# Optimization experiments

Hardware: AMD Instinct MI355X
Metric: run time of the kernel (lower is better)

## Reference

```python
import jax, jax.numpy as jnp
import numpy as np

B, K, D, S, E = 256, 512, 64, 100000, 20000  # batch, knowledge_n, low_dim, student_n, exer_n


def setup_inputs() -> dict:
    key = jax.random.key(0)
    ks = jax.random.split(key, 10)
    stu_id = jax.random.randint(ks[0], (B,), 0, S)
    exer_id = jax.random.randint(ks[1], (B,), 0, E)
    kn_emb = jax.random.uniform(ks[2], (B, K), dtype=jnp.float32)
    # learned parameters (xavier-ish scale)
    stu_table = jax.random.normal(ks[3], (S, D), dtype=jnp.float32) * 0.05
    exer_table = jax.random.normal(ks[4], (E, D), dtype=jnp.float32) * 0.05
    kn_table = jax.random.normal(ks[5], (K, D), dtype=jnp.float32) * 0.05
    W1 = jax.random.normal(ks[6], (K, K + D), dtype=jnp.float32) * (2.0 / (2 * K + D)) ** 0.5
    W2 = jax.random.normal(ks[7], (K, K + D), dtype=jnp.float32) * (2.0 / (2 * K + D)) ** 0.5
    W3 = jax.random.normal(ks[8], (1, K), dtype=jnp.float32) * (2.0 / (K + 1)) ** 0.5
    b3 = jnp.zeros((1,), dtype=jnp.float32)
    return {"stu_id": stu_id, "exer_id": exer_id, "kn_emb": kn_emb,
            "stu_table": stu_table, "exer_table": exer_table, "kn_table": kn_table,
            "W1": W1, "W2": W2, "W3": W3, "b3": b3}


def reference(stu_id, exer_id, kn_emb, stu_table, exer_table, kn_table, W1, W2, W3, b3):
    k = kn_table.shape[0]  # knowledge_n
    # sigmoid(stu_emb @ kn_table.T): (B, K) per-concept proficiency / difficulty
    stu = jax.nn.sigmoid(stu_table[stu_id] @ kn_table.T)
    exer = jax.nn.sigmoid(exer_table[exer_id] @ kn_table.T)
    # Linear on cat([repeated stu/exer vec, kn_vector]) decomposes: split W into
    # the first K columns (acting on the batch vector, constant over the K axis)
    # and the last D columns (acting on kn_table, constant over batch).
    pref = jax.nn.sigmoid((stu @ W1[:, :k].T)[:, None, :] + (kn_table @ W1[:, k:].T)[None, :, :])  # (B,K,K)
    diff = jax.nn.sigmoid((exer @ W2[:, :k].T)[:, None, :] + (kn_table @ W2[:, k:].T)[None, :, :])  # (B,K,K)
    o = jax.nn.sigmoid(jnp.einsum('bkn,n->bk', pref - diff, W3[0]) + b3)  # (B,K)
    sum_out = jnp.sum(o * kn_emb, axis=1, keepdims=True)  # (B,1)
    count = jnp.sum(kn_emb, axis=1, keepdims=True)
    return sum_out / count
```

## Files before the change

kernel.cpp:

```cpp
#include <hip/hip_runtime.h>

#define B_ 256
#define K_ 512
#define D_ 64
#define KD_ 576
#define LOG2E 1.44269504088896340736f

typedef float v2f __attribute__((ext_vector_type(2)));
typedef float v4f __attribute__((ext_vector_type(4)));
typedef short bf16x8 __attribute__((ext_vector_type(8)));
typedef float f32x16 __attribute__((ext_vector_type(16)));

#define ZERO16 {0.f,0.f,0.f,0.f,0.f,0.f,0.f,0.f,0.f,0.f,0.f,0.f,0.f,0.f,0.f,0.f}

__device__ __forceinline__ float fexp2(float x) {
#if __has_builtin(__builtin_amdgcn_exp2f)
    return __builtin_amdgcn_exp2f(x);
#else
    float r; asm("v_exp_f32 %0, %1" : "=v"(r) : "v"(x)); return r;
#endif
}
__device__ __forceinline__ float frcp(float x) {
#if __has_builtin(__builtin_amdgcn_rcpf)
    return __builtin_amdgcn_rcpf(x);
#else
    float r; asm("v_rcp_f32 %0, %1" : "=v"(r) : "v"(x)); return r;
#endif
}
__device__ __forceinline__ float fsig(float x) {
    return frcp(1.0f + fexp2(-LOG2E * x));
}
__device__ __forceinline__ ushort f2bf(float f) {
    union { float f; unsigned u; } v; v.f = f;
    return (ushort)((v.u + 0x7FFFu + ((v.u >> 16) & 1u)) >> 16);
}
__device__ __forceinline__ bf16x8 ldcvt8(const float* p) {
    float4 a = *(const float4*)p;
    float4 b = *(const float4*)(p + 4);
    bf16x8 r;
    r[0] = (short)f2bf(a.x); r[1] = (short)f2bf(a.y);
    r[2] = (short)f2bf(a.z); r[3] = (short)f2bf(a.w);
    r[4] = (short)f2bf(b.x); r[5] = (short)f2bf(b.y);
    r[6] = (short)f2bf(b.z); r[7] = (short)f2bf(b.w);
    return r;
}

__global__ void __launch_bounds__(256) kS(const int* __restrict__ sid,
                                          const int* __restrict__ eid,
                                          const float* __restrict__ stu_t,
                                          const float* __restrict__ exer_t,
                                          const float* __restrict__ kn_t,
                                          ushort* __restrict__ Sbu) {
    const int bid = blockIdx.x, t = threadIdx.x;
    const int l = t & 63, w = t >> 6;
    const int dk = (l >> 5) * 8;
    const int tab = bid >> 5, bt = (bid >> 3) & 3, nt = bid & 7;
    const int b0 = bt * 64, n0 = nt * 64;
    const int brow = b0 + (w & 1) * 32 + (l & 31);
    const int ncol = n0 + (w >> 1) * 32 + (l & 31);
    const int id = (tab ? eid : sid)[brow];
    const float* ar = (tab ? exer_t : stu_t) + (size_t)id * D_;
    const float* br = kn_t + (size_t)ncol * D_;
    f32x16 acc = ZERO16;
#pragma unroll
    for (int kk = 0; kk < 4; kk++) {
        bf16x8 a = ldcvt8(ar + kk * 16 + dk);
        bf16x8 b = ldcvt8(br + kk * 16 + dk);
        acc = __builtin_amdgcn_mfma_f32_32x32x16_bf16(a, b, acc, 0, 0, 0);
    }
    ushort* So = Sbu + (size_t)tab * B_ * K_;
#pragma unroll
    for (int r = 0; r < 16; r++) {
        const int row = (r & 3) + 8 * (r >> 2) + 4 * (l >> 5);
        So[(size_t)(b0 + (w & 1) * 32 + row) * K_ + ncol] = f2bf(fsig(acc[r]));
    }
}

__global__ void __launch_bounds__(256) kEF(const ushort* __restrict__ Sbu,
                                           const float* __restrict__ W1,
                                           const float* __restrict__ W2,
                                           const float* __restrict__ kn_t,
                                           float* __restrict__ E,
                                           float* __restrict__ FT1,
                                           float* __restrict__ FT2) {
    __shared__ float shm[4224];
    const int bid = blockIdx.x, t = threadIdx.x;
    const int l = t & 63, w = t >> 6;
    if (bid < 256) {
        const int mat = bid >> 7, bt = (bid >> 4) & 7, nt = bid & 15;
        const int b0 = bt * 32, n0 = nt * 32;
        const int arow = b0 + (l & 31);
        const int nrow = n0 + (l & 31);
        const int koff = w * 128 + (l >> 5) * 8;
        const short* Sp = (const short*)Sbu + (size_t)(mat * B_ + arow) * K_ + koff;
        const float* Wp = (mat ? W2 : W1) + (size_t)nrow * KD_ + koff;
        f32x16 acc = ZERO16;
#pragma unroll
        for (int kk = 0; kk < 8; kk++) {
            bf16x8 a = *(const bf16x8*)(Sp + kk * 16);
            bf16x8 b = ldcvt8(Wp + kk * 16);
            acc = __builtin_amdgcn_mfma_f32_32x32x16_bf16(a, b, acc, 0, 0, 0);
        }
#pragma unroll
        for (int r = 0; r < 16; r++) {
            const int row = (r & 3) + 8 * (r >> 2) + 4 * (l >> 5);
            shm[w * 1056 + row * 33 + (l & 31)] = acc[r];
        }
        __syncthreads();
#pragma unroll
        for (int i = 0; i < 4; i++) {
            const int o = i * 256 + t;
            const int row = (o >> 5) & 31, col = o & 31;
            const float v = shm[row * 33 + col] + shm[1056 + row * 33 + col]
                          + shm[2112 + row * 33 + col] + shm[3168 + row * 33 + col];
            E[(size_t)mat * B_ * K_ + (size_t)(b0 + row) * K_ + n0 + col]
                = fexp2(-LOG2E * v);
        }
    } else {
        const int fid = bid - 256;
        const int mat = fid >> 6, kt = (fid >> 3) & 7, nt = fid & 7;
        const int k0 = kt * 64, n0 = nt * 64;
        const int krow = k0 + (w & 1) * 32 + (l & 31);
        const int ncol = n0 + (w >> 1) * 32 + (l & 31);
        const int dk = (l >> 5) * 8;
        const float* Wm = mat ? W2 : W1;
        const float* ar = kn_t + (size_t)krow * D_;
        const float* br = Wm + (size_t)ncol * KD_ + K_;
        f32x16 acc = ZERO16;
#pragma unroll
        for (int kk = 0; kk < 4; kk++) {
            bf16x8 a = ldcvt8(ar + kk * 16 + dk);
            bf16x8 b = ldcvt8(br + kk * 16 + dk);
            acc = __builtin_amdgcn_mfma_f32_32x32x16_bf16(a, b, acc, 0, 0, 0);
        }
        const int nl_ = (w >> 1) * 32 + (l & 31);
#pragma unroll
        for (int r = 0; r < 16; r++) {
            const int row = (r & 3) + 8 * (r >> 2) + 4 * (l >> 5);
            shm[nl_ * 65 + (w & 1) * 32 + row] = fexp2(-LOG2E * acc[r]);
        }
        __syncthreads();
        float* Fo = mat ? FT2 : FT1;
#pragma unroll
        for (int i = 0; i < 16; i++) {
            const int q = i * 256 + t;
            const int r_ = q >> 6, c_ = q & 63;
            Fo[(size_t)(n0 + r_) * K_ + k0 + c_] = shm[r_ * 65 + c_];
        }
    }
}

__global__ void __launch_bounds__(512) kMain(const float* __restrict__ FT1,
                                             const float* __restrict__ FT2,
                                             const float* __restrict__ Ebase,
                                             const float* __restrict__ W3,
                                             float* __restrict__ pPart) {
    __shared__ float lds[4352];
    const int t = threadIdx.x;
    const int l = t & 63, w = t >> 6;
    const int kg = blockIdx.x, bg = blockIdx.y, ns = blockIdx.z;
    const int b0 = bg * 8;
    const int k = kg * 64 + l;

#pragma unroll
    for (int c = 0; c < 2; c++) {
        const int combo = w * 2 + c;
        const int mat = combo >> 3, b = combo & 7;
        const float* src = Ebase + (size_t)mat * B_ * K_ + (size_t)(b0 + b) * K_
                         + ns * 256;
#pragma unroll
        for (int j = 0; j < 4; j++) {
            const int nl = j * 64 + l;
            lds[mat * 2048 + nl * 8 + b] = src[nl];
        }
    }
    if (t < 256) lds[4096 + t] = W3[ns * 256 + t];
    __syncthreads();

    const int nbase = w * 32;
    const float* f1p = FT1 + (size_t)(ns * 256 + nbase) * K_ + k;
    const float* f2p = FT2 + (size_t)(ns * 256 + nbase) * K_ + k;

    v2f acc0 = {0.f, 0.f}, acc1 = {0.f, 0.f}, acc2 = {0.f, 0.f}, acc3 = {0.f, 0.f};

#pragma unroll 4
    for (int nl = 0; nl < 32; nl++) {
        const float f1 = f1p[(size_t)nl * K_];
        const float f2 = f2p[(size_t)nl * K_];
        const int n = nbase + nl;
        const float w3n = lds[4096 + n];
        const v4f e1a = *(const v4f*)&lds[n * 8];
        const v4f e1b = *(const v4f*)&lds[n * 8 + 4];
        const v4f e2a = *(const v4f*)&lds[2048 + n * 8];
        const v4f e2b = *(const v4f*)&lds[2048 + n * 8 + 4];
        {
            const v2f e1 = {e1a.x, e1a.y}, e2 = {e2a.x, e2a.y};
            const v2f pd = e1 * f1 + 1.0f, qd = e2 * f2 + 1.0f;
            const v2f den = pd * qd;
            v2f rc; rc.x = frcp(den.x); rc.y = frcp(den.y);
            acc0 += ((qd - pd) * w3n) * rc;
        }
        {
            const v2f e1 = {e1a.z, e1a.w}, e2 = {e2a.z, e2a.w};
            const v2f pd = e1 * f1 + 1.0f, qd = e2 * f2 + 1.0f;
            const v2f den = pd * qd;
            v2f rc; rc.x = frcp(den.x); rc.y = frcp(den.y);
            acc1 += ((qd - pd) * w3n) * rc;
        }
        {
            const v2f e1 = {e1b.x, e1b.y}, e2 = {e2b.x, e2b.y};
            const v2f pd = e1 * f1 + 1.0f, qd = e2 * f2 + 1.0f;
            const v2f den = pd * qd;
            v2f rc; rc.x = frcp(den.x); rc.y = frcp(den.y);
            acc2 += ((qd - pd) * w3n) * rc;
        }
        {
            const v2f e1 = {e1b.z, e1b.w}, e2 = {e2b.z, e2b.w};
            const v2f pd = e1 * f1 + 1.0f, qd = e2 * f2 + 1.0f;
            const v2f den = pd * qd;
            v2f rc; rc.x = frcp(den.x); rc.y = frcp(den.y);
            acc3 += ((qd - pd) * w3n) * rc;
        }
    }

    __syncthreads();
    {
        float* sa = lds + w * 512 + l * 8;
        *(v2f*)(sa + 0) = acc0;
        *(v2f*)(sa + 2) = acc1;
        *(v2f*)(sa + 4) = acc2;
        *(v2f*)(sa + 6) = acc3;
    }
    __syncthreads();
    float s = 0.f;
#pragma unroll
    for (int ww = 0; ww < 8; ww++) s += lds[ww * 512 + l * 8 + w];
    pPart[(((size_t)ns * 32 + bg) * 8 + w) * K_ + kg * 64 + l] = s;
}

__global__ void __launch_bounds__(256) kFin(const float* __restrict__ pPart,
                                            const float* __restrict__ kn_emb,
                                            const float* __restrict__ b3,
                                            float* __restrict__ out) {
    const int t = threadIdx.x, l = t & 63, w = t >> 6;
    const int b = blockIdx.x * 4 + w;
    const int bg = b >> 3, bi = b & 7;
    const float b3v = b3[0];
    const float* p0 = pPart + (((size_t)0 * 32 + bg) * 8 + bi) * K_;
    const float* p1 = pPart + (((size_t)1 * 32 + bg) * 8 + bi) * K_;
    const float* ke = kn_emb + (size_t)b * K_;
    float num = 0.f, den = 0.f;
#pragma unroll
    for (int c = 0; c < 8; c++) {
        const int kk = c * 64 + l;
        const float s = p0[kk] + p1[kk];
        const float kv = ke[kk];
        num = fmaf(fsig(s + b3v), kv, num);
        den += kv;
    }
#pragma unroll
    for (int off = 32; off; off >>= 1) {
        num += __shfl_xor(num, off, 64);
        den += __shfl_xor(den, off, 64);
    }
    if (l == 0) out[b] = num / den;
}

extern "C" void kernel_launch(void* const* d_in, const int* in_sizes, int n_in,
                              void* d_out, int out_size, void* d_ws, size_t ws_size,
                              hipStream_t stream) {
    const int*   stu_id     = (const int*)d_in[0];
    const int*   exer_id    = (const int*)d_in[1];
    const float* kn_emb     = (const float*)d_in[2];
    const float* stu_table  = (const float*)d_in[3];
    const float* exer_table = (const float*)d_in[4];
    const float* kn_table   = (const float*)d_in[5];
    const float* W1         = (const float*)d_in[6];
    const float* W2         = (const float*)d_in[7];
    const float* W3         = (const float*)d_in[8];
    const float* b3         = (const float*)d_in[9];
    float* out = (float*)d_out;

    float* ws = (float*)d_ws;
    float* FT1      = ws;
    float* FT2      = FT1 + (size_t)K_ * K_;
    float* E        = FT2 + (size_t)K_ * K_;
    ushort* Sbu     = (ushort*)(E + 2 * (size_t)B_ * K_);
    float* pPart    = (float*)(Sbu + 2 * (size_t)B_ * K_);

    kS<<<64, 256, 0, stream>>>(stu_id, exer_id, stu_table, exer_table,
                               kn_table, Sbu);
    kEF<<<384, 256, 0, stream>>>(Sbu, W1, W2, kn_table, E, FT1, FT2);
    kMain<<<dim3(8, 32, 2), 512, 0, stream>>>(FT1, FT2, E, W3, pPart);
    kFin<<<64, 256, 0, stream>>>(pPart, kn_emb, b3, out);
}
```

Baseline: 36.52 us.

## Fuse S and E GEMMs into one kernel and recompute F tiles inside main kernel

Result: slower. 46.18 us (+26.4%).

```diff
diff --git a/kernel.cpp b/kernel.cpp
--- a/kernel.cpp
+++ b/kernel.cpp
@@ -45,154 +45,139 @@
     return r;
 }
 
-__global__ void __launch_bounds__(256) kS(const int* __restrict__ sid,
-                                          const int* __restrict__ eid,
-                                          const float* __restrict__ stu_t,
-                                          const float* __restrict__ exer_t,
-                                          const float* __restrict__ kn_t,
-                                          ushort* __restrict__ Sbu) {
+__global__ void __launch_bounds__(256) kE2(const int* __restrict__ sid,
+                                           const int* __restrict__ eid,
+                                           const float* __restrict__ stu_t,
+                                           const float* __restrict__ exer_t,
+                                           const float* __restrict__ kn_t,
+                                           const float* __restrict__ W1,
+                                           const float* __restrict__ W2,
+                                           float* __restrict__ E) {
+    __shared__ ushort S_lds[32 * 512];
+    __shared__ float red[4 * 32 * 33];
+    __shared__ int ids[32];
     const int bid = blockIdx.x, t = threadIdx.x;
     const int l = t & 63, w = t >> 6;
-    const int dk = (l >> 5) * 8;
-    const int tab = bid >> 5, bt = (bid >> 3) & 3, nt = bid & 7;
-    const int b0 = bt * 64, n0 = nt * 64;
-    const int brow = b0 + (w & 1) * 32 + (l & 31);
-    const int ncol = n0 + (w >> 1) * 32 + (l & 31);
-    const int id = (tab ? eid : sid)[brow];
-    const float* ar = (tab ? exer_t : stu_t) + (size_t)id * D_;
-    const float* br = kn_t + (size_t)ncol * D_;
-    f32x16 acc = ZERO16;
-#pragma unroll
-    for (int kk = 0; kk < 4; kk++) {
-        bf16x8 a = ldcvt8(ar + kk * 16 + dk);
-        bf16x8 b = ldcvt8(br + kk * 16 + dk);
-        acc = __builtin_amdgcn_mfma_f32_32x32x16_bf16(a, b, acc, 0, 0, 0);
-    }
-    ushort* So = Sbu + (size_t)tab * B_ * K_;
-#pragma unroll
-    for (int r = 0; r < 16; r++) {
-        const int row = (r & 3) + 8 * (r >> 2) + 4 * (l >> 5);
-        So[(size_t)(b0 + (w & 1) * 32 + row) * K_ + ncol] = f2bf(fsig(acc[r]));
-    }
-}
-
-__global__ void __launch_bounds__(256) kEF(const ushort* __restrict__ Sbu,
-                                           const float* __restrict__ W1,
-                                           const float* __restrict__ W2,
-                                           const float* __restrict__ kn_t,
-                                           float* __restrict__ E,
-                                           float* __restrict__ FT1,
-                                           float* __restrict__ FT2) {
-    __shared__ float shm[4224];
-    const int bid = blockIdx.x, t = threadIdx.x;
-    const int l = t & 63, w = t >> 6;
-    if (bid < 256) {
-        const int mat = bid >> 7, bt = (bid >> 4) & 7, nt = bid & 15;
-        const int b0 = bt * 32, n0 = nt * 32;
-        const int arow = b0 + (l & 31);
-        const int nrow = n0 + (l & 31);
-        const int koff = w * 128 + (l >> 5) * 8;
-        const short* Sp = (const short*)Sbu + (size_t)(mat * B_ + arow) * K_ + koff;
-        const float* Wp = (mat ? W2 : W1) + (size_t)nrow * KD_ + koff;
+    const int mat = bid >> 7, bt = (bid >> 4) & 7, nt = bid & 15;
+    const int b0 = bt * 32, n0 = nt * 32;
+    if (t < 32) ids[t] = (mat ? eid : sid)[b0 + t];
+    __syncthreads();
+
+    {
+        const float* tab = mat ? exer_t : stu_t;
+        const float* ar = tab + (size_t)ids[l & 31] * D_ + (l >> 5) * 8;
+        const bf16x8 a0 = ldcvt8(ar),      a1 = ldcvt8(ar + 16),
+                     a2 = ldcvt8(ar + 32), a3 = ldcvt8(ar + 48);
+#pragma unroll
+        for (int tt = 0; tt < 4; tt++) {
+            const int ncol = w * 128 + tt * 32 + (l & 31);
+            const float* br = kn_t + (size_t)ncol * D_ + (l >> 5) * 8;
+            f32x16 acc = ZERO16;
+            acc = __builtin_amdgcn_mfma_f32_32x32x16_bf16(a0, ldcvt8(br),      acc, 0, 0, 0);
+            acc = __builtin_amdgcn_mfma_f32_32x32x16_bf16(a1, ldcvt8(br + 16), acc, 0, 0, 0);
+            acc = __builtin_amdgcn_mfma_f32_32x32x16_bf16(a2, ldcvt8(br + 32), acc, 0, 0, 0);
+            acc = __builtin_amdgcn_mfma_f32_32x32x16_bf16(a3, ldcvt8(br + 48), acc, 0, 0, 0);
+#pragma unroll
+            for (int r = 0; r < 16; r++) {
+                const int row = (r & 3) + 8 * (r >> 2) + 4 * (l >> 5);
+                const int byte = row * 1024 + ((ncol * 2) ^ ((row & 7) << 4));
+                *(ushort*)((char*)S_lds + byte) = f2bf(fsig(acc[r]));
+            }
+        }
+    }
+    __syncthreads();
+
+    {
+        const int row = l & 31;
+        const int swz = (row & 7) << 4;
+        const int kbase = w * 128 + (l >> 5) * 8;
+        const float* wr = (mat ? W2 : W1) + (size_t)(n0 + (l & 31)) * KD_ + kbase;
         f32x16 acc = ZERO16;
 #pragma unroll
         for (int kk = 0; kk < 8; kk++) {
-            bf16x8 a = *(const bf16x8*)(Sp + kk * 16);
-            bf16x8 b = ldcvt8(Wp + kk * 16);
+            const int kel = kbase + kk * 16;
+            bf16x8 a = *(const bf16x8*)((const char*)S_lds + row * 1024 + ((kel * 2) ^ swz));
+            bf16x8 b = ldcvt8(wr + kk * 16);
             acc = __builtin_amdgcn_mfma_f32_32x32x16_bf16(a, b, acc, 0, 0, 0);
         }
 #pragma unroll
         for (int r = 0; r < 16; r++) {
-            const int row = (r & 3) + 8 * (r >> 2) + 4 * (l >> 5);
-            shm[w * 1056 + row * 33 + (l & 31)] = acc[r];
-        }
-        __syncthreads();
-#pragma unroll
-        for (int i = 0; i < 4; i++) {
-            const int o = i * 256 + t;
-            const int row = (o >> 5) & 31, col = o & 31;
-            const float v = shm[row * 33 + col] + shm[1056 + row * 33 + col]
-                          + shm[2112 + row * 33 + col] + shm[3168 + row * 33 + col];
-            E[(size_t)mat * B_ * K_ + (size_t)(b0 + row) * K_ + n0 + col]
-                = fexp2(-LOG2E * v);
-        }
-    } else {
-        const int fid = bid - 256;
-        const int mat = fid >> 6, kt = (fid >> 3) & 7, nt = fid & 7;
-        const int k0 = kt * 64, n0 = nt * 64;
-        const int krow = k0 + (w & 1) * 32 + (l & 31);
-        const int ncol = n0 + (w >> 1) * 32 + (l & 31);
-        const int dk = (l >> 5) * 8;
-        const float* Wm = mat ? W2 : W1;
-        const float* ar = kn_t + (size_t)krow * D_;
-        const float* br = Wm + (size_t)ncol * KD_ + K_;
-        f32x16 acc = ZERO16;
-#pragma unroll
-        for (int kk = 0; kk < 4; kk++) {
-            bf16x8 a = ldcvt8(ar + kk * 16 + dk);
-            bf16x8 b = ldcvt8(br + kk * 16 + dk);
-            acc = __builtin_amdgcn_mfma_f32_32x32x16_bf16(a, b, acc, 0, 0, 0);
-        }
-        const int nl_ = (w >> 1) * 32 + (l & 31);
-#pragma unroll
-        for (int r = 0; r < 16; r++) {
-            const int row = (r & 3) + 8 * (r >> 2) + 4 * (l >> 5);
-            shm[nl_ * 65 + (w & 1) * 32 + row] = fexp2(-LOG2E * acc[r]);
-        }
-        __syncthreads();
-        float* Fo = mat ? FT2 : FT1;
-#pragma unroll
-        for (int i = 0; i < 16; i++) {
-            const int q = i * 256 + t;
-            const int r_ = q >> 6, c_ = q & 63;
-            Fo[(size_t)(n0 + r_) * K_ + k0 + c_] = shm[r_ * 65 + c_];
-        }
-    }
-}
-
-__global__ void __launch_bounds__(512) kMain(const float* __restrict__ FT1,
-                                             const float* __restrict__ FT2,
+            const int rowc = (r & 3) + 8 * (r >> 2) + 4 * (l >> 5);
+            red[w * 1056 + rowc * 33 + (l & 31)] = acc[r];
+        }
+    }
+    __syncthreads();
+#pragma unroll
+    for (int i = 0; i < 4; i++) {
+        const int o = i * 256 + t;
+        const int row = (o >> 5) & 31, col = o & 31;
+        const float v = red[row * 33 + col] + red[1056 + row * 33 + col]
+                      + red[2112 + row * 33 + col] + red[3168 + row * 33 + col];
+        E[(size_t)mat * B_ * K_ + (size_t)(b0 + row) * K_ + n0 + col]
+            = fexp2(-LOG2E * v);
+    }
+}
+
+__global__ void __launch_bounds__(512) kMain(const float* __restrict__ kn_t,
+                                             const float* __restrict__ W1,
+                                             const float* __restrict__ W2,
                                              const float* __restrict__ Ebase,
                                              const float* __restrict__ W3,
                                              float* __restrict__ pPart) {
-    __shared__ float lds[4352];
-    const int t = threadIdx.x;
-    const int l = t & 63, w = t >> 6;
+    __shared__ float lds[18816];
+    const int t = threadIdx.x, l = t & 63, w = t >> 6;
     const int kg = blockIdx.x, bg = blockIdx.y, ns = blockIdx.z;
     const int b0 = bg * 8;
-    const int k = kg * 64 + l;
-
-#pragma unroll
-    for (int c = 0; c < 2; c++) {
-        const int combo = w * 2 + c;
-        const int mat = combo >> 3, b = combo & 7;
-        const float* src = Ebase + (size_t)mat * B_ * K_ + (size_t)(b0 + b) * K_
-                         + ns * 256;
-#pragma unroll
-        for (int j = 0; j < 4; j++) {
-            const int nl = j * 64 + l;
-            lds[mat * 2048 + nl * 8 + b] = src[nl];
-        }
-    }
-    if (t < 256) lds[4096 + t] = W3[ns * 256 + t];
-    __syncthreads();
-
-    const int nbase = w * 32;
-    const float* f1p = FT1 + (size_t)(ns * 256 + nbase) * K_ + k;
-    const float* f2p = FT2 + (size_t)(ns * 256 + nbase) * K_ + k;
+
+    {
+        const int tid0 = w * 2;
+        const int mat = tid0 >> 3, kt = (tid0 >> 2) & 1;
+        const int krow = kg * 64 + kt * 32 + (l & 31);
+        const float* ar = kn_t + (size_t)krow * D_ + (l >> 5) * 8;
+        const bf16x8 a0 = ldcvt8(ar),      a1 = ldcvt8(ar + 16),
+                     a2 = ldcvt8(ar + 32), a3 = ldcvt8(ar + 48);
+        const float* Wm = mat ? W2 : W1;
+#pragma unroll
+        for (int c = 0; c < 2; c++) {
+            const int nt = (tid0 + c) & 3;
+            const int nrow = ns * 128 + nt * 32 + (l & 31);
+            const float* br = Wm + (size_t)nrow * KD_ + K_ + (l >> 5) * 8;
+            f32x16 acc = ZERO16;
+            acc = __builtin_amdgcn_mfma_f32_32x32x16_bf16(a0, ldcvt8(br),      acc, 0, 0, 0);
+            acc = __builtin_amdgcn_mfma_f32_32x32x16_bf16(a1, ldcvt8(br + 16), acc, 0, 0, 0);
+            acc = __builtin_amdgcn_mfma_f32_32x32x16_bf16(a2, ldcvt8(br + 32), acc, 0, 0, 0);
+            acc = __builtin_amdgcn_mfma_f32_32x32x16_bf16(a3, ldcvt8(br + 48), acc, 0, 0, 0);
+            const int nl = nt * 32 + (l & 31);
+#pragma unroll
+            for (int r = 0; r < 16; r++) {
+                const int kl = kt * 32 + (r & 3) + 8 * (r >> 2) + 4 * (l >> 5);
+                lds[mat * 8320 + nl * 65 + kl] = fexp2(-LOG2E * acc[r]);
+            }
+        }
+    }
+    {
+        const int i = t * 4;
+        const int mat = i >> 10, r2 = i & 1023, nl = r2 >> 3, bq = r2 & 7;
+        const float* Em = Ebase + (size_t)mat * B_ * K_ + (size_t)(b0 + bq) * K_
+                        + ns * 128 + nl;
+        v4f ev; ev.x = Em[0]; ev.y = Em[K_]; ev.z = Em[2 * K_]; ev.w = Em[3 * K_];
+        *(v4f*)&lds[16640 + i] = ev;
+    }
+    if (t < 128) lds[18688 + t] = W3[ns * 128 + t];
+    __syncthreads();
 
     v2f acc0 = {0.f, 0.f}, acc1 = {0.f, 0.f}, acc2 = {0.f, 0.f}, acc3 = {0.f, 0.f};
-
+    const int nbase = w * 16;
 #pragma unroll 4
-    for (int nl = 0; nl < 32; nl++) {
-        const float f1 = f1p[(size_t)nl * K_];
-        const float f2 = f2p[(size_t)nl * K_];
+    for (int nl = 0; nl < 16; nl++) {
         const int n = nbase + nl;
-        const float w3n = lds[4096 + n];
-        const v4f e1a = *(const v4f*)&lds[n * 8];
-        const v4f e1b = *(const v4f*)&lds[n * 8 + 4];
-        const v4f e2a = *(const v4f*)&lds[2048 + n * 8];
-        const v4f e2b = *(const v4f*)&lds[2048 + n * 8 + 4];
+        const float f1 = lds[n * 65 + l];
+        const float f2 = lds[8320 + n * 65 + l];
+        const float w3n = lds[18688 + n];
+        const v4f e1a = *(const v4f*)&lds[16640 + n * 8];
+        const v4f e1b = *(const v4f*)&lds[16640 + n * 8 + 4];
+        const v4f e2a = *(const v4f*)&lds[17664 + n * 8];
+        const v4f e2b = *(const v4f*)&lds[17664 + n * 8 + 4];
         {
             const v2f e1 = {e1a.x, e1a.y}, e2 = {e2a.x, e2a.y};
             const v2f pd = e1 * f1 + 1.0f, qd = e2 * f2 + 1.0f;
@@ -225,16 +210,16 @@
 
     __syncthreads();
     {
-        float* sa = lds + w * 512 + l * 8;
-        *(v2f*)(sa + 0) = acc0;
-        *(v2f*)(sa + 2) = acc1;
-        *(v2f*)(sa + 4) = acc2;
-        *(v2f*)(sa + 6) = acc3;
+        const int base = w * 576 + l * 9;
+        lds[base + 0] = acc0.x; lds[base + 1] = acc0.y;
+        lds[base + 2] = acc1.x; lds[base + 3] = acc1.y;
+        lds[base + 4] = acc2.x; lds[base + 5] = acc2.y;
+        lds[base + 6] = acc3.x; lds[base + 7] = acc3.y;
     }
     __syncthreads();
     float s = 0.f;
 #pragma unroll
-    for (int ww = 0; ww < 8; ww++) s += lds[ww * 512 + l * 8 + w];
+    for (int ww = 0; ww < 8; ww++) s += lds[ww * 576 + l * 9 + w];
     pPart[(((size_t)ns * 32 + bg) * 8 + w) * K_ + kg * 64 + l] = s;
 }
 
@@ -248,14 +233,16 @@
     const float b3v = b3[0];
     const float* p0 = pPart + (((size_t)0 * 32 + bg) * 8 + bi) * K_;
     const float* p1 = pPart + (((size_t)1 * 32 + bg) * 8 + bi) * K_;
+    const float* p2 = pPart + (((size_t)2 * 32 + bg) * 8 + bi) * K_;
+    const float* p3 = pPart + (((size_t)3 * 32 + bg) * 8 + bi) * K_;
     const float* ke = kn_emb + (size_t)b * K_;
     float num = 0.f, den = 0.f;
 #pragma unroll
     for (int c = 0; c < 8; c++) {
         const int kk = c * 64 + l;
-        const float s = p0[kk] + p1[kk];
+        const float sv = p0[kk] + p1[kk] + p2[kk] + p3[kk];
         const float kv = ke[kk];
-        num = fmaf(fsig(s + b3v), kv, num);
+        num = fmaf(fsig(sv + b3v), kv, num);
         den += kv;
     }
 #pragma unroll
@@ -282,15 +269,11 @@
     float* out = (float*)d_out;
 
     float* ws = (float*)d_ws;
-    float* FT1      = ws;
-    float* FT2      = FT1 + (size_t)K_ * K_;
-    float* E        = FT2 + (size_t)K_ * K_;
-    ushort* Sbu     = (ushort*)(E + 2 * (size_t)B_ * K_);
-    float* pPart    = (float*)(Sbu + 2 * (size_t)B_ * K_);
-
-    kS<<<64, 256, 0, stream>>>(stu_id, exer_id, stu_table, exer_table,
-                               kn_table, Sbu);
-    kEF<<<384, 256, 0, stream>>>(Sbu, W1, W2, kn_table, E, FT1, FT2);
-    kMain<<<dim3(8, 32, 2), 512, 0, stream>>>(FT1, FT2, E, W3, pPart);
+    float* E     = ws;
+    float* pPart = E + 2 * (size_t)B_ * K_;
+
+    kE2<<<256, 256, 0, stream>>>(stu_id, exer_id, stu_table, exer_table,
+                                 kn_table, W1, W2, E);
+    kMain<<<dim3(8, 32, 4), 512, 0, stream>>>(kn_table, W1, W2, E, W3, pPart);
     kFin<<<64, 256, 0, stream>>>(pPart, kn_emb, b3, out);
 }
```

## Rebalance kernel stages and retile main kernel for vector FT loads

Applied to the files above, without the earlier changes.

Measured after the change: 38.16 us. 4.5% more time.

```diff
diff --git a/kernel.cpp b/kernel.cpp
--- a/kernel.cpp
+++ b/kernel.cpp
@@ -45,84 +45,47 @@
     return r;
 }
 
-__global__ void __launch_bounds__(256) kS(const int* __restrict__ sid,
-                                          const int* __restrict__ eid,
-                                          const float* __restrict__ stu_t,
-                                          const float* __restrict__ exer_t,
-                                          const float* __restrict__ kn_t,
-                                          ushort* __restrict__ Sbu) {
+__global__ void __launch_bounds__(256) kSF(const int* __restrict__ sid,
+                                           const int* __restrict__ eid,
+                                           const float* __restrict__ stu_t,
+                                           const float* __restrict__ exer_t,
+                                           const float* __restrict__ kn_t,
+                                           const float* __restrict__ W1,
+                                           const float* __restrict__ W2,
+                                           ushort* __restrict__ Sbu,
+                                           float* __restrict__ FT1,
+                                           float* __restrict__ FT2) {
+    __shared__ float shm[64 * 65];
     const int bid = blockIdx.x, t = threadIdx.x;
     const int l = t & 63, w = t >> 6;
     const int dk = (l >> 5) * 8;
-    const int tab = bid >> 5, bt = (bid >> 3) & 3, nt = bid & 7;
-    const int b0 = bt * 64, n0 = nt * 64;
-    const int brow = b0 + (w & 1) * 32 + (l & 31);
-    const int ncol = n0 + (w >> 1) * 32 + (l & 31);
-    const int id = (tab ? eid : sid)[brow];
-    const float* ar = (tab ? exer_t : stu_t) + (size_t)id * D_;
-    const float* br = kn_t + (size_t)ncol * D_;
-    f32x16 acc = ZERO16;
-#pragma unroll
-    for (int kk = 0; kk < 4; kk++) {
-        bf16x8 a = ldcvt8(ar + kk * 16 + dk);
-        bf16x8 b = ldcvt8(br + kk * 16 + dk);
-        acc = __builtin_amdgcn_mfma_f32_32x32x16_bf16(a, b, acc, 0, 0, 0);
-    }
-    ushort* So = Sbu + (size_t)tab * B_ * K_;
-#pragma unroll
-    for (int r = 0; r < 16; r++) {
-        const int row = (r & 3) + 8 * (r >> 2) + 4 * (l >> 5);
-        So[(size_t)(b0 + (w & 1) * 32 + row) * K_ + ncol] = f2bf(fsig(acc[r]));
-    }
-}
-
-__global__ void __launch_bounds__(256) kEF(const ushort* __restrict__ Sbu,
-                                           const float* __restrict__ W1,
-                                           const float* __restrict__ W2,
-                                           const float* __restrict__ kn_t,
-                                           float* __restrict__ E,
-                                           float* __restrict__ FT1,
-                                           float* __restrict__ FT2) {
-    __shared__ float shm[4224];
-    const int bid = blockIdx.x, t = threadIdx.x;
-    const int l = t & 63, w = t >> 6;
-    if (bid < 256) {
-        const int mat = bid >> 7, bt = (bid >> 4) & 7, nt = bid & 15;
-        const int b0 = bt * 32, n0 = nt * 32;
-        const int arow = b0 + (l & 31);
-        const int nrow = n0 + (l & 31);
-        const int koff = w * 128 + (l >> 5) * 8;
-        const short* Sp = (const short*)Sbu + (size_t)(mat * B_ + arow) * K_ + koff;
-        const float* Wp = (mat ? W2 : W1) + (size_t)nrow * KD_ + koff;
+    if (bid < 64) {
+        const int tab = bid >> 5, bt = (bid >> 3) & 3, nt = bid & 7;
+        const int b0 = bt * 64, n0 = nt * 64;
+        const int brow = b0 + (w & 1) * 32 + (l & 31);
+        const int ncol = n0 + (w >> 1) * 32 + (l & 31);
+        const int id = (tab ? eid : sid)[brow];
+        const float* ar = (tab ? exer_t : stu_t) + (size_t)id * D_;
+        const float* br = kn_t + (size_t)ncol * D_;
         f32x16 acc = ZERO16;
 #pragma unroll
-        for (int kk = 0; kk < 8; kk++) {
-            bf16x8 a = *(const bf16x8*)(Sp + kk * 16);
-            bf16x8 b = ldcvt8(Wp + kk * 16);
+        for (int kk = 0; kk < 4; kk++) {
+            bf16x8 a = ldcvt8(ar + kk * 16 + dk);
+            bf16x8 b = ldcvt8(br + kk * 16 + dk);
             acc = __builtin_amdgcn_mfma_f32_32x32x16_bf16(a, b, acc, 0, 0, 0);
         }
+        ushort* So = Sbu + (size_t)tab * B_ * K_;
 #pragma unroll
         for (int r = 0; r < 16; r++) {
             const int row = (r & 3) + 8 * (r >> 2) + 4 * (l >> 5);
-            shm[w * 1056 + row * 33 + (l & 31)] = acc[r];
-        }
-        __syncthreads();
-#pragma unroll
-        for (int i = 0; i < 4; i++) {
-            const int o = i * 256 + t;
-            const int row = (o >> 5) & 31, col = o & 31;
-            const float v = shm[row * 33 + col] + shm[1056 + row * 33 + col]
-                          + shm[2112 + row * 33 + col] + shm[3168 + row * 33 + col];
-            E[(size_t)mat * B_ * K_ + (size_t)(b0 + row) * K_ + n0 + col]
-                = fexp2(-LOG2E * v);
+            So[(size_t)(b0 + (w & 1) * 32 + row) * K_ + ncol] = f2bf(fsig(acc[r]));
         }
     } else {
-        const int fid = bid - 256;
+        const int fid = bid - 64;
         const int mat = fid >> 6, kt = (fid >> 3) & 7, nt = fid & 7;
         const int k0 = kt * 64, n0 = nt * 64;
         const int krow = k0 + (w & 1) * 32 + (l & 31);
         const int ncol = n0 + (w >> 1) * 32 + (l & 31);
-        const int dk = (l >> 5) * 8;
         const float* Wm = mat ? W2 : W1;
         const float* ar = kn_t + (size_t)krow * D_;
         const float* br = Wm + (size_t)ncol * KD_ + K_;
@@ -147,6 +110,44 @@
             const int r_ = q >> 6, c_ = q & 63;
             Fo[(size_t)(n0 + r_) * K_ + k0 + c_] = shm[r_ * 65 + c_];
         }
+    }
+}
+
+__global__ void __launch_bounds__(256) kE(const ushort* __restrict__ Sbu,
+                                          const float* __restrict__ W1,
+                                          const float* __restrict__ W2,
+                                          float* __restrict__ E) {
+    __shared__ float shm[4224];
+    const int bid = blockIdx.x, t = threadIdx.x;
+    const int l = t & 63, w = t >> 6;
+    const int mat = bid >> 7, bt = (bid >> 4) & 7, nt = bid & 15;
+    const int b0 = bt * 32, n0 = nt * 32;
+    const int arow = b0 + (l & 31);
+    const int nrow = n0 + (l & 31);
+    const int koff = w * 128 + (l >> 5) * 8;
+    const short* Sp = (const short*)Sbu + (size_t)(mat * B_ + arow) * K_ + koff;
+    const float* Wp = (mat ? W2 : W1) + (size_t)nrow * KD_ + koff;
+    f32x16 acc = ZERO16;
+#pragma unroll
+    for (int kk = 0; kk < 8; kk++) {
+        bf16x8 a = *(const bf16x8*)(Sp + kk * 16);
+        bf16x8 b = ldcvt8(Wp + kk * 16);
+        acc = __builtin_amdgcn_mfma_f32_32x32x16_bf16(a, b, acc, 0, 0, 0);
+    }
+#pragma unroll
+    for (int r = 0; r < 16; r++) {
+        const int row = (r & 3) + 8 * (r >> 2) + 4 * (l >> 5);
+        shm[w * 1056 + row * 33 + (l & 31)] = acc[r];
+    }
+    __syncthreads();
+#pragma unroll
+    for (int i = 0; i < 4; i++) {
+        const int o = i * 256 + t;
+        const int row = (o >> 5) & 31, col = o & 31;
+        const float v = shm[row * 33 + col] + shm[1056 + row * 33 + col]
+                      + shm[2112 + row * 33 + col] + shm[3168 + row * 33 + col];
+        E[(size_t)mat * B_ * K_ + (size_t)(b0 + row) * K_ + n0 + col]
+            = fexp2(-LOG2E * v);
     }
 }
 
@@ -155,87 +156,87 @@
                                              const float* __restrict__ Ebase,
                                              const float* __restrict__ W3,
                                              float* __restrict__ pPart) {
-    __shared__ float lds[4352];
-    const int t = threadIdx.x;
-    const int l = t & 63, w = t >> 6;
-    const int kg = blockIdx.x, bg = blockIdx.y, ns = blockIdx.z;
-    const int b0 = bg * 8;
-    const int k = kg * 64 + l;
-
-#pragma unroll
-    for (int c = 0; c < 2; c++) {
-        const int combo = w * 2 + c;
-        const int mat = combo >> 3, b = combo & 7;
-        const float* src = Ebase + (size_t)mat * B_ * K_ + (size_t)(b0 + b) * K_
-                         + ns * 256;
-#pragma unroll
-        for (int j = 0; j < 4; j++) {
-            const int nl = j * 64 + l;
-            lds[mat * 2048 + nl * 8 + b] = src[nl];
-        }
-    }
-    if (t < 256) lds[4096 + t] = W3[ns * 256 + t];
+    __shared__ float es[2][32][20];
+    __shared__ float w3s[32];
+    __shared__ float sacc[4][64][20];
+    const int t = threadIdx.x, l = t & 63, w = t >> 6;
+    const int kg = blockIdx.x, bG = blockIdx.y, ns = blockIdx.z;
+    const int b0 = bG * 16, n0 = ns * 32;
+    const int k = kg * 256 + l * 4;
+
+#pragma unroll
+    for (int it = 0; it < 2; it++) {
+        const int idx = it * 512 + t;
+        const int mat = idx >> 9, r = idx & 511, bl = r >> 5, nl = r & 31;
+        es[mat][nl][bl] = Ebase[(size_t)mat * B_ * K_ + (size_t)(b0 + bl) * K_ + n0 + nl];
+    }
+    if (t < 32) w3s[t] = W3[n0 + t];
     __syncthreads();
 
-    const int nbase = w * 32;
-    const float* f1p = FT1 + (size_t)(ns * 256 + nbase) * K_ + k;
-    const float* f2p = FT2 + (size_t)(ns * 256 + nbase) * K_ + k;
-
-    v2f acc0 = {0.f, 0.f}, acc1 = {0.f, 0.f}, acc2 = {0.f, 0.f}, acc3 = {0.f, 0.f};
+    const int bg = w & 3, nh = w >> 2;
+    const int wb0 = bg * 4;
+    const float* f1p = FT1 + (size_t)(n0 + nh * 16) * K_ + k;
+    const float* f2p = FT2 + (size_t)(n0 + nh * 16) * K_ + k;
+
+    v4f acc0 = {0.f,0.f,0.f,0.f}, acc1 = {0.f,0.f,0.f,0.f};
+    v4f acc2 = {0.f,0.f,0.f,0.f}, acc3 = {0.f,0.f,0.f,0.f};
 
 #pragma unroll 4
-    for (int nl = 0; nl < 32; nl++) {
-        const float f1 = f1p[(size_t)nl * K_];
-        const float f2 = f2p[(size_t)nl * K_];
-        const int n = nbase + nl;
-        const float w3n = lds[4096 + n];
-        const v4f e1a = *(const v4f*)&lds[n * 8];
-        const v4f e1b = *(const v4f*)&lds[n * 8 + 4];
-        const v4f e2a = *(const v4f*)&lds[2048 + n * 8];
-        const v4f e2b = *(const v4f*)&lds[2048 + n * 8 + 4];
-        {
-            const v2f e1 = {e1a.x, e1a.y}, e2 = {e2a.x, e2a.y};
-            const v2f pd = e1 * f1 + 1.0f, qd = e2 * f2 + 1.0f;
-            const v2f den = pd * qd;
-            v2f rc; rc.x = frcp(den.x); rc.y = frcp(den.y);
+    for (int nl = 0; nl < 16; nl++) {
+        const int n = nh * 16 + nl;
+        const v4f f1 = *(const v4f*)(f1p + (size_t)nl * K_);
+        const v4f f2 = *(const v4f*)(f2p + (size_t)nl * K_);
+        const float w3n = w3s[n];
+        const v4f e1 = *(const v4f*)&es[0][n][wb0];
+        const v4f e2 = *(const v4f*)&es[1][n][wb0];
+        {
+            const v4f pd = e1.x * f1 + 1.0f, qd = e2.x * f2 + 1.0f;
+            const v4f den = pd * qd;
+            v4f rc; rc.x = frcp(den.x); rc.y = frcp(den.y);
+            rc.z = frcp(den.z); rc.w = frcp(den.w);
             acc0 += ((qd - pd) * w3n) * rc;
         }
         {
-            const v2f e1 = {e1a.z, e1a.w}, e2 = {e2a.z, e2a.w};
-            const v2f pd = e1 * f1 + 1.0f, qd = e2 * f2 + 1.0f;
-            const v2f den = pd * qd;
-            v2f rc; rc.x = frcp(den.x); rc.y = frcp(den.y);
+            const v4f pd = e1.y * f1 + 1.0f, qd = e2.y * f2 + 1.0f;
+            const v4f den = pd * qd;
+            v4f rc; rc.x = frcp(den.x); rc.y = frcp(den.y);
+            rc.z = frcp(den.z); rc.w = frcp(den.w);
             acc1 += ((qd - pd) * w3n) * rc;
         }
         {
-            const v2f e1 = {e1b.x, e1b.y}, e2 = {e2b.x, e2b.y};
-            const v2f pd = e1 * f1 + 1.0f, qd = e2 * f2 + 1.0f;
-            const v2f den = pd * qd;
-            v2f rc; rc.x = frcp(den.x); rc.y = frcp(den.y);
+            const v4f pd = e1.z * f1 + 1.0f, qd = e2.z * f2 + 1.0f;
+            const v4f den = pd * qd;
+            v4f rc; rc.x = frcp(den.x); rc.y = frcp(den.y);
+            rc.z = frcp(den.z); rc.w = frcp(den.w);
             acc2 += ((qd - pd) * w3n) * rc;
         }
         {
-            const v2f e1 = {e1b.z, e1b.w}, e2 = {e2b.z, e2b.w};
-            const v2f pd = e1 * f1 + 1.0f, qd = e2 * f2 + 1.0f;
-            const v2f den = pd * qd;
-            v2f rc; rc.x = frcp(den.x); rc.y = frcp(den.y);
+            const v4f pd = e1.w * f1 + 1.0f, qd = e2.w * f2 + 1.0f;
+            const v4f den = pd * qd;
+            v4f rc; rc.x = frcp(den.x); rc.y = frcp(den.y);
+            rc.z = frcp(den.z); rc.w = frcp(den.w);
             acc3 += ((qd - pd) * w3n) * rc;
         }
     }
 
+    if (nh == 0) {
+        *(v4f*)&sacc[bg][l][0]  = acc0;
+        *(v4f*)&sacc[bg][l][4]  = acc1;
+        *(v4f*)&sacc[bg][l][8]  = acc2;
+        *(v4f*)&sacc[bg][l][12] = acc3;
+    }
     __syncthreads();
-    {
-        float* sa = lds + w * 512 + l * 8;
-        *(v2f*)(sa + 0) = acc0;
-        *(v2f*)(sa + 2) = acc1;
-        *(v2f*)(sa + 4) = acc2;
-        *(v2f*)(sa + 6) = acc3;
-    }
-    __syncthreads();
-    float s = 0.f;
-#pragma unroll
-    for (int ww = 0; ww < 8; ww++) s += lds[ww * 512 + l * 8 + w];
-    pPart[(((size_t)ns * 32 + bg) * 8 + w) * K_ + kg * 64 + l] = s;
+    if (nh == 1) {
+        const v4f o0 = acc0 + *(const v4f*)&sacc[bg][l][0];
+        const v4f o1 = acc1 + *(const v4f*)&sacc[bg][l][4];
+        const v4f o2 = acc2 + *(const v4f*)&sacc[bg][l][8];
+        const v4f o3 = acc3 + *(const v4f*)&sacc[bg][l][12];
+        float* po = pPart + ((size_t)ns * B_ + b0 + wb0) * K_ + k;
+        *(v4f*)(po)          = o0;
+        *(v4f*)(po + K_)     = o1;
+        *(v4f*)(po + 2 * K_) = o2;
+        *(v4f*)(po + 3 * K_) = o3;
+    }
 }
 
 __global__ void __launch_bounds__(256) kFin(const float* __restrict__ pPart,
@@ -244,18 +245,18 @@
                                             float* __restrict__ out) {
     const int t = threadIdx.x, l = t & 63, w = t >> 6;
     const int b = blockIdx.x * 4 + w;
-    const int bg = b >> 3, bi = b & 7;
     const float b3v = b3[0];
-    const float* p0 = pPart + (((size_t)0 * 32 + bg) * 8 + bi) * K_;
-    const float* p1 = pPart + (((size_t)1 * 32 + bg) * 8 + bi) * K_;
     const float* ke = kn_emb + (size_t)b * K_;
     float num = 0.f, den = 0.f;
 #pragma unroll
     for (int c = 0; c < 8; c++) {
         const int kk = c * 64 + l;
-        const float s = p0[kk] + p1[kk];
+        float sv = 0.f;
+#pragma unroll
+        for (int s = 0; s < 16; s++)
+            sv += pPart[((size_t)s * B_ + b) * K_ + kk];
         const float kv = ke[kk];
-        num = fmaf(fsig(s + b3v), kv, num);
+        num = fmaf(fsig(sv + b3v), kv, num);
         den += kv;
     }
 #pragma unroll
@@ -282,15 +283,15 @@
     float* out = (float*)d_out;
 
     float* ws = (float*)d_ws;
-    float* FT1      = ws;
-    float* FT2      = FT1 + (size_t)K_ * K_;
-    float* E        = FT2 + (size_t)K_ * K_;
-    ushort* Sbu     = (ushort*)(E + 2 * (size_t)B_ * K_);
-    float* pPart    = (float*)(Sbu + 2 * (size_t)B_ * K_);
-
-    kS<<<64, 256, 0, stream>>>(stu_id, exer_id, stu_table, exer_table,
-                               kn_table, Sbu);
-    kEF<<<384, 256, 0, stream>>>(Sbu, W1, W2, kn_table, E, FT1, FT2);
-    kMain<<<dim3(8, 32, 2), 512, 0, stream>>>(FT1, FT2, E, W3, pPart);
+    float* FT1   = ws;
+    float* FT2   = FT1 + (size_t)K_ * K_;
+    float* E     = FT2 + (size_t)K_ * K_;
+    ushort* Sbu  = (ushort*)(E + 2 * (size_t)B_ * K_);
+    float* pPart = (float*)(Sbu + 2 * (size_t)B_ * K_);
+
+    kSF<<<192, 256, 0, stream>>>(stu_id, exer_id, stu_table, exer_table,
+                                 kn_table, W1, W2, Sbu, FT1, FT2);
+    kE<<<256, 256, 0, stream>>>(Sbu, W1, W2, E);
+    kMain<<<dim3(2, 16, 16), 512, 0, stream>>>(FT1, FT2, E, W3, pPart);
     kFin<<<64, 256, 0, stream>>>(pPart, kn_emb, b3, out);
 }
```
